# Optimization experiments

Measured on AMD Instinct MI355X. Metric: run time of the kernel, lower is better.

Reference implementation:

```python
import jax, jax.numpy as jnp
import numpy as np

B = 32
CH = 64
BAND = 16384
NOISE_SAMPLES = 64
NOISE_FRAMES = BAND // NOISE_SAMPLES          # 256
NOISE_COEFFS = NOISE_FRAMES // 2 + 1          # 129
NOISE_STEP = NOISE_FRAMES // 2                # 128


def setup_inputs() -> dict:
    key = jax.random.key(0)
    ks = jax.random.split(key, 6)
    def w(k, o, i):
        return jax.random.normal(k, (o, i), jnp.float32) / np.sqrt(i).astype(np.float32)
    x = jax.random.normal(ks[0], (B, CH, BAND), jnp.float32)
    # white noise uniform(-1, 1), generated in torch forward; here a fixed input for determinism
    white_noise = jax.random.uniform(ks[1], (B, BAND), jnp.float32) * 2.0 - 1.0
    return {
        "x": x,
        "amp_w": w(ks[2], CH, CH), "amp_b": jnp.zeros((CH,), jnp.float32),
        "freq_w": w(ks[3], CH, CH), "freq_b": jnp.zeros((CH,), jnp.float32),
        "noise_w": w(ks[4], NOISE_COEFFS, CH), "noise_b": jnp.zeros((NOISE_COEFFS,), jnp.float32),
        "noise_factor": jnp.array(1e-5, jnp.float32),
        "white_noise": white_noise,
    }


def _avg_pool_same(y, k=64, p=32):
    # F.avg_pool1d(y, 64, 1, 32)[..., :-1] with count_include_pad=True
    s = jax.lax.reduce_window(y, 0.0, jax.lax.add, (1, 1, k), (1, 1, 1),
                              ((0, 0), (0, 0), (p, p)))
    return (s / k)[..., : y.shape[-1]]


def _noise_bank2(spec, white):
    # spec: [B, M, S] per-frame rFFT magnitudes; filter white noise frame-wise, overlap-add
    b, m, s = spec.shape
    win = (m - 1) * 2          # 256
    hop = win // 2             # 128
    total = hop * s            # == BAND
    noise = jnp.pad(white, ((0, 0), (0, hop)))
    idx = jnp.arange(s)[:, None] * hop + jnp.arange(win)[None, :]
    frames = noise[:, idx]
    nf = jnp.fft.rfft(frames, norm="ortho")             # [B, S, M]
    filt = nf * jnp.transpose(spec, (0, 2, 1))          # apply magnitudes
    audio = jnp.fft.irfft(filt, n=win, norm="ortho")
    a = audio[:, :, :hop]
    tail = audio[:, :, hop:]
    ola = a.at[:, 1:, :].add(tail[:, :-1, :])
    return ola.reshape(b, 1, total)


def reference(x, amp_w, amp_b, freq_w, freq_b, noise_w, noise_b, noise_factor, white_noise):
    b, c, t = x.shape
    conv1x1 = lambda w_, b_: jnp.einsum("oc,bct->bot", w_, x) + b_[None, :, None]
    # noise branch
    n = jnp.clip(conv1x1(noise_w, noise_b), 0.0, 1.0)                 # [B, 129, T]
    n = n.reshape(b, NOISE_COEFFS, t // NOISE_STEP, NOISE_STEP).mean(-1)  # avg_pool k=s=128
    nb = _noise_bank2(n, white_noise) * noise_factor                  # [B, 1, T]
    # amp/freq oscillator branch (computed but DISCARDED by the original forward)
    amp = _avg_pool_same(jnp.clip(conv1x1(amp_w, amp_b), 0.0, 1.0))
    freq = _avg_pool_same(jnp.clip(conv1x1(freq_w, freq_b), 0.0, 1.0))
    osc = jnp.sin(jnp.cumsum(freq, axis=-1)) * amp                    # noqa: F841 (dead in source)
    out = jnp.mean(x, axis=1, keepdims=True) + nb
    return out
```

## Files before the change

### kernel.cpp

```cpp
#include <hip/hip_runtime.h>
#include <stdint.h>

#define B_    32
#define CH    64
#define T_    16384
#define NC    129
#define NFRM  128
#define QPAD  136
#define MROWS 144
#define FPB   8

typedef __attribute__((ext_vector_type(4))) float f32x4;
typedef __attribute__((ext_vector_type(4))) int   i32x4;
typedef __attribute__((ext_vector_type(8))) short bf16x8;

__device__ f32x4 llvm_amdgcn_raw_buffer_load_v4f32(i32x4 rsrc, int voffset, int soffset, int aux) __asm("llvm.amdgcn.raw.buffer.load.v4f32");

__device__ __forceinline__ unsigned short f2bs(float f) {
  union { float f; unsigned u; } v; v.f = f;
  unsigned r = (v.u + 0x7FFFu + ((v.u >> 16) & 1u)) >> 16;
  return (unsigned short)r;
}
__device__ __forceinline__ float b2f(unsigned short s) {
  union { float f; unsigned u; } v; v.u = ((unsigned)s) << 16; return v.f;
}
__device__ __forceinline__ unsigned pk2(float lo, float hi) {
  return __builtin_amdgcn_perm(__float_as_uint(hi), __float_as_uint(lo), 0x07060302u);
}
__device__ __forceinline__ i32x4 make_srsrc_wave(const void* p) {
  unsigned long long a = (unsigned long long)p;
  i32x4 r;
  r[0] = __builtin_amdgcn_readfirstlane((int)(unsigned)a);
  r[1] = __builtin_amdgcn_readfirstlane(((int)(unsigned)(a >> 32)) & 0xFFFF);
  r[2] = -1;
  r[3] = 0x00020000;
  return r;
}
__device__ __forceinline__ float dpp_sum16(float v) {
  float t;
  t = __int_as_float(__builtin_amdgcn_update_dpp(0, __float_as_int(v), 0x121, 0xF, 0xF, false)); v += t;
  t = __int_as_float(__builtin_amdgcn_update_dpp(0, __float_as_int(v), 0x122, 0xF, 0xF, false)); v += t;
  t = __int_as_float(__builtin_amdgcn_update_dpp(0, __float_as_int(v), 0x124, 0xF, 0xF, false)); v += t;
  t = __int_as_float(__builtin_amdgcn_update_dpp(0, __float_as_int(v), 0x128, 0xF, 0xF, false)); v += t;
  return v;
}
__device__ __forceinline__ void bar_lgkm() {
  asm volatile("s_waitcnt lgkmcnt(0)" ::: "memory");
  __builtin_amdgcn_s_barrier();
  asm volatile("" ::: "memory");
}

__global__ __launch_bounds__(256) void k0_setup(
    unsigned short* __restrict__ T1, unsigned short* __restrict__ T2,
    const float* __restrict__ nw, const float* __restrict__ nb,
    unsigned short* __restrict__ wb_ws, float* __restrict__ bias_ws) {
  int bid = blockIdx.x;
  if (bid < 64) {
    int g = bid * 256 + threadIdx.x;
    int base = g * 8;
    int tab = base >> 16;
    int off = base & 65535;
    int row = off >> 8, col0 = off & 255;
    const float w0 = 6.283185307179586f / 256.f;
    bf16x8 pk;
#pragma unroll
    for (int e = 0; e < 8; ++e) {
      int cq = col0 + e;
      float v;
      if (tab == 0) {
        int q = row, m = cq;
        int idx = (q <= 128) ? ((q * m) & 255) : (((q - 128) * m + 192) & 255);
        v = cosf((float)idx * w0);
      } else {
        int n = row, q = cq;
        float c = (q == 0 || q == 128) ? 1.f : 2.f;
        int idx = (q <= 128) ? ((q * n) & 255) : (((q - 128) * n + 192) & 255);
        v = c * cosf((float)idx * w0);
      }
      pk[e] = (short)f2bs(v);
    }
    *(bf16x8*)((tab ? T2 : T1) + off) = pk;
  } else {
    int t = (bid - 64) * 256 + threadIdx.x;
    if (t < MROWS * 8) {
      int q = t >> 3, o = t & 7;
      bf16x8 pk;
#pragma unroll
      for (int e = 0; e < 8; ++e) {
        unsigned short v = 0;
        if (q < NC)       v = f2bs(nw[q * 64 + o * 8 + e]);
        else if (q == 129) v = 0x3F80;
        pk[e] = (short)v;
      }
      *(bf16x8*)(wb_ws + q * 64 + o * 8) = pk;
    }
    if (t < MROWS) bias_ws[t] = (t < NC) ? nb[t] : 0.f;
  }
}

__global__ __launch_bounds__(512, 4) void k1_spec_mean(
    const float* __restrict__ x, const unsigned short* __restrict__ wb_ws,
    const float* __restrict__ bias_ws, float* __restrict__ out,
    unsigned short* __restrict__ spec_ws) {
  __shared__ __align__(16) unsigned short xbT[2][128 * 64];

  const int tid = threadIdx.x;
  const int w = tid >> 6, lane = tid & 63;
  const int l15 = lane & 15, l4 = lane >> 4;
  const int g = tid >> 5, c16 = tid & 31;
  const int b = blockIdx.y;
  const int j0 = blockIdx.x * FPB;

  const int ntile = (w == 0) ? 2 : 1;
  bf16x8 wf[2][2];
  f32x4  bfr[2];
#pragma unroll
  for (int ti = 0; ti < 2; ++ti) {
    if (ti < ntile) {
      int tile = (ti == 0) ? w : 8;
#pragma unroll
      for (int kt = 0; kt < 2; ++kt)
        wf[ti][kt] = *(const bf16x8*)(wb_ws + (tile * 16 + l15) * 64 + kt * 32 + l4 * 8);
      bfr[ti] = *(const f32x4*)(bias_ws + tile * 16 + l4 * 4);
    }
  }

  i32x4 rx = make_srsrc_wave(x + (size_t)b * CH * T_);
  const int vxbase = (g * 4 * T_ + c16 * 4) * 4;

  f32x4 r[4];
#pragma unroll
  for (int it = 0; it < 4; ++it)
    r[it] = llvm_amdgcn_raw_buffer_load_v4f32(rx, vxbase + j0 * 512, it * (T_ * 4), 0);

#pragma unroll 2
  for (int f = 0; f < FPB; ++f) {
    const int j = j0 + f;
    char* xb = (char*)xbT + (f & 1) * 16384;

    {
      const int o8 = g >> 1, h = g & 1;
#pragma unroll
      for (int e = 0; e < 4; ++e) {
        int t = c16 * 4 + e;
        unsigned a = (unsigned)(t * 128 + o8 * 16 + h * 8);
        a ^= (unsigned)(((t ^ (t >> 3)) & 7) << 4);
        uint2 dv = make_uint2(pk2(r[0][e], r[1][e]), pk2(r[2][e], r[3][e]));
        *(uint2*)(xb + a) = dv;
      }
    }
    if (f < FPB - 1) {
#pragma unroll
      for (int it = 0; it < 4; ++it)
        r[it] = llvm_amdgcn_raw_buffer_load_v4f32(rx, vxbase + (j + 1) * 512, it * (T_ * 4), 0);
    }
    bar_lgkm();

    f32x4 sum[2];
    sum[0] = (f32x4){0.f, 0.f, 0.f, 0.f};
    sum[1] = (f32x4){0.f, 0.f, 0.f, 0.f};
#pragma unroll
    for (int tt = 0; tt < 8; ++tt) {
      int t = tt * 16 + l15;
      unsigned a0 = (unsigned)(t * 128 + l4 * 16);
      a0 ^= (unsigned)(((t ^ (t >> 3)) & 7) << 4);
      bf16x8 xb0 = *(const bf16x8*)(xb + a0);
      bf16x8 xb1 = *(const bf16x8*)(xb + (a0 ^ 64));
#pragma unroll
      for (int ti = 0; ti < 2; ++ti) {
        if (ti < ntile) {
          f32x4 acc = bfr[ti];
          acc = __builtin_amdgcn_mfma_f32_16x16x32_bf16(wf[ti][0], xb0, acc, 0, 0, 0);
          acc = __builtin_amdgcn_mfma_f32_16x16x32_bf16(wf[ti][1], xb1, acc, 0, 0, 0);
          if (ti == 1 && l4 == 0)
            out[(size_t)b * T_ + (size_t)j * 128 + tt * 16 + l15] = acc[1] * (1.f / 64.f);
#pragma unroll
          for (int rr = 0; rr < 4; ++rr)
            sum[ti][rr] += __builtin_amdgcn_fmed3f(acc[rr], 0.f, 1.f);
        }
      }
    }
    unsigned short* sp = spec_ws + ((size_t)b * NFRM + j) * QPAD;
#pragma unroll
    for (int ti = 0; ti < 2; ++ti) {
      if (ti < ntile) {
        int tile = (ti == 0) ? w : 8;
        float s0 = dpp_sum16(sum[ti][0]) * (1.f / 128.f);
        float s1 = dpp_sum16(sum[ti][1]) * (1.f / 128.f);
        float s2 = dpp_sum16(sum[ti][2]) * (1.f / 128.f);
        float s3 = dpp_sum16(sum[ti][3]) * (1.f / 128.f);
        if (l15 == 0) {
          uint2 pv = make_uint2(pk2(s0, s1), pk2(s2, s3));
          *(uint2*)(sp + tile * 16 + l4 * 4) = pv;
        }
      }
    }
  }
}

__global__ __launch_bounds__(512) void k2_noise(
    const float* __restrict__ white, const unsigned short* __restrict__ spec_ws,
    const unsigned short* __restrict__ T1, const unsigned short* __restrict__ T2,
    const float* __restrict__ nf_p, float* __restrict__ out) {
  __shared__ __align__(16) unsigned short wn[4224];
  __shared__ __align__(16) unsigned short spec_l[32 * QPAD];
  __shared__ __align__(16) unsigned short G[32 * 256];
  __shared__ __align__(16) unsigned short audio[256 * 33];

  const int c = blockIdx.x, b = blockIdx.y;
  const int jb = c * 16 - 1;
  const int tid = threadIdx.x;
  const int lane = tid & 63, w = tid >> 6;
  const int l15 = lane & 15, l4 = lane >> 4;

  for (int rc = tid; rc < 528; rc += 512) {
    int g0 = jb * 128 + rc * 8;
    bf16x8 pk;
    if (rc < 288 && (unsigned)g0 < (unsigned)T_) {
      const float* wp = white + (size_t)b * T_ + g0;
      union { unsigned u[4]; bf16x8 h; } t;
#pragma unroll
      for (int p = 0; p < 4; ++p) t.u[p] = pk2(wp[2 * p], wp[2 * p + 1]);
      pk = t.h;
    } else {
#pragma unroll
      for (int e = 0; e < 8; ++e) pk[e] = 0;
    }
    unsigned a = rc * 16;
    a ^= ((a >> 8) & 7) << 4;
    *(bf16x8*)((char*)wn + a) = pk;
  }
  for (int ec = tid; ec < 32 * 17; ec += 512) {
    int s = ec / 17, cr = ec % 17;
    int jj = jb + s;
    uint4 vv = make_uint4(0u, 0u, 0u, 0u);
    if (s < 17 && (unsigned)jj < 128u)
      vv = *(const uint4*)(spec_ws + ((size_t)b * NFRM + jj) * QPAD + cr * 8);
    *(uint4*)(spec_l + s * QPAD + cr * 8) = vv;
  }
  __syncthreads();

  const f32x4 fz = {0.f, 0.f, 0.f, 0.f};
  f32x4 acc[2][2];
#pragma unroll
  for (int mi = 0; mi < 2; ++mi)
#pragma unroll
    for (int nt = 0; nt < 2; ++nt) acc[mi][nt] = fz;
#pragma unroll
  for (int kt = 0; kt < 8; ++kt) {
    bf16x8 bfr[2];
#pragma unroll
    for (int nt = 0; nt < 2; ++nt) {
      int s = nt * 16 + l15;
      unsigned a = s * 256 + kt * 64 + l4 * 16;
      a ^= ((a >> 8) & 7) << 4;
      bfr[nt] = *(const bf16x8*)((const char*)wn + a);
    }
#pragma unroll
    for (int mi = 0; mi < 2; ++mi) {
      int q = (2 * w + mi) * 16 + l15;
      bf16x8 afr = *(const bf16x8*)(T1 + q * 256 + kt * 32 + l4 * 8);
#pragma unroll
      for (int nt = 0; nt < 2; ++nt)
        acc[mi][nt] = __builtin_amdgcn_mfma_f32_16x16x32_bf16(afr, bfr[nt], acc[mi][nt], 0, 0, 0);
    }
  }
#pragma unroll
  for (int mi = 0; mi < 2; ++mi) {
    int qbase = (2 * w + mi) * 16 + l4 * 4;
#pragma unroll
    for (int nt = 0; nt < 2; ++nt) {
      int s = nt * 16 + l15;
#pragma unroll
      for (int rp = 0; rp < 2; ++rp) {
        int q0 = qbase + rp * 2;
        int kk0 = (q0 <= 128) ? q0 : q0 - 128;
        int kk1 = (q0 + 1 <= 128) ? q0 + 1 : q0 - 127;
        float s0 = b2f(spec_l[s * QPAD + kk0]);
        float s1 = b2f(spec_l[s * QPAD + kk1]);
        unsigned pw = pk2(acc[mi][nt][rp * 2] * s0, acc[mi][nt][rp * 2 + 1] * s1);
        unsigned a = s * 512 + q0 * 2;
        a ^= ((a >> 9) & 7) << 4;
        *(unsigned*)((char*)G + a) = pw;
      }
    }
  }
  __syncthreads();

  f32x4 acc2[2][2];
#pragma unroll
  for (int mi = 0; mi < 2; ++mi)
#pragma unroll
    for (int nt = 0; nt < 2; ++nt) acc2[mi][nt] = fz;
#pragma unroll
  for (int kt = 0; kt < 8; ++kt) {
    bf16x8 bfr[2];
#pragma unroll
    for (int nt = 0; nt < 2; ++nt) {
      int s = nt * 16 + l15;
      unsigned a = s * 512 + kt * 64 + l4 * 16;
      a ^= ((a >> 9) & 7) << 4;
      bfr[nt] = *(const bf16x8*)((const char*)G + a);
    }
#pragma unroll
    for (int mi = 0; mi < 2; ++mi) {
      int n = (2 * w + mi) * 16 + l15;
      bf16x8 afr = *(const bf16x8*)(T2 + n * 256 + kt * 32 + l4 * 8);
#pragma unroll
      for (int nt = 0; nt < 2; ++nt)
        acc2[mi][nt] = __builtin_amdgcn_mfma_f32_16x16x32_bf16(afr, bfr[nt], acc2[mi][nt], 0, 0, 0);
    }
  }
#pragma unroll
  for (int mi = 0; mi < 2; ++mi)
#pragma unroll
    for (int nt = 0; nt < 2; ++nt)
#pragma unroll
      for (int r = 0; r < 4; ++r) {
        int n = (2 * w + mi) * 16 + l4 * 4 + r;
        int s = nt * 16 + l15;
        audio[n * 33 + s] = f2bs(acc2[mi][nt][r]);
      }
  __syncthreads();

  const float cf = nf_p[0] * (1.f / 256.f);
  {
    int t0 = tid * 4;
    int n = t0 & 127, jl = t0 >> 7;
    int s1 = jl + 1;
    size_t o = (size_t)b * T_ + (size_t)c * 2048 + t0;
    f32x4 ov = *(f32x4*)(out + o);
#pragma unroll
    for (int e = 0; e < 4; ++e) {
      float a1 = b2f(audio[(n + e) * 33 + s1]);
      float a2 = b2f(audio[(n + e + 128) * 33 + jl]);
      ov[e] += cf * (a1 + a2);
    }
    *(f32x4*)(out + o) = ov;
  }
}

extern "C" void kernel_launch(void* const* d_in, const int* in_sizes, int n_in,
                              void* d_out, int out_size, void* d_ws, size_t ws_size,
                              hipStream_t stream) {
  (void)in_sizes; (void)n_in; (void)out_size; (void)ws_size;
  const float* x            = (const float*)d_in[0];
  const float* noise_w      = (const float*)d_in[5];
  const float* noise_b      = (const float*)d_in[6];
  const float* noise_factor = (const float*)d_in[7];
  const float* white        = (const float*)d_in[8];
  float* out = (float*)d_out;

  unsigned short* T1    = (unsigned short*)d_ws;
  unsigned short* T2    = T1 + 65536;
  unsigned short* spec  = T2 + 65536;
  unsigned short* wb_ws = spec + (size_t)B_ * NFRM * QPAD;
  float*          bias_ws = (float*)(wb_ws + MROWS * 64);

  k0_setup<<<69, 256, 0, stream>>>(T1, T2, noise_w, noise_b, wb_ws, bias_ws);
  k1_spec_mean<<<dim3(NFRM / FPB, B_), 512, 0, stream>>>(x, wb_ws, bias_ws, out, spec);
  k2_noise<<<dim3(8, B_), 512, 0, stream>>>(white, spec, T1, T2, noise_factor, out);
}
```

Measured before the change: 44.82 us.

## Halve k2 chunk size for more blocks and deepen k1 prefetch to two frames

The noise kernel now processes 8 frames per block instead of 16, which doubles the grid to 512 blocks and shrinks shared memory and per-wave accumulators to one N tile. The aim is better occupancy and spreading across CUs, at the cost of reloading more T1/T2 table fragments and the one-frame halo per block. The spec/mean kernel is fully unrolled with two register buffers so global loads for x are issued two frames ahead, hiding more load latency at the cost of higher register pressure.

```diff
diff --git a/kernel.cpp b/kernel.cpp
--- a/kernel.cpp
+++ b/kernel.cpp
@@ -9,6 +9,7 @@
 #define QPAD  136
 #define MROWS 144
 #define FPB   8
+#define CHK   8
 
 typedef __attribute__((ext_vector_type(4))) float f32x4;
 typedef __attribute__((ext_vector_type(4))) int   i32x4;
@@ -88,7 +89,7 @@
 #pragma unroll
       for (int e = 0; e < 8; ++e) {
         unsigned short v = 0;
-        if (q < NC)       v = f2bs(nw[q * 64 + o * 8 + e]);
+        if (q < NC)        v = f2bs(nw[q * 64 + o * 8 + e]);
         else if (q == 129) v = 0x3F80;
         pk[e] = (short)v;
       }
@@ -127,96 +128,110 @@
 
   i32x4 rx = make_srsrc_wave(x + (size_t)b * CH * T_);
   const int vxbase = (g * 4 * T_ + c16 * 4) * 4;
-
-  f32x4 r[4];
+  const int o8 = g >> 1, hh = g & 1;
+
+  f32x4 rA[4], rB[4];
 #pragma unroll
   for (int it = 0; it < 4; ++it)
-    r[it] = llvm_amdgcn_raw_buffer_load_v4f32(rx, vxbase + j0 * 512, it * (T_ * 4), 0);
-
-#pragma unroll 2
-  for (int f = 0; f < FPB; ++f) {
-    const int j = j0 + f;
-    char* xb = (char*)xbT + (f & 1) * 16384;
-
-    {
-      const int o8 = g >> 1, h = g & 1;
-#pragma unroll
-      for (int e = 0; e < 4; ++e) {
-        int t = c16 * 4 + e;
-        unsigned a = (unsigned)(t * 128 + o8 * 16 + h * 8);
-        a ^= (unsigned)(((t ^ (t >> 3)) & 7) << 4);
-        uint2 dv = make_uint2(pk2(r[0][e], r[1][e]), pk2(r[2][e], r[3][e]));
-        *(uint2*)(xb + a) = dv;
-      }
-    }
-    if (f < FPB - 1) {
-#pragma unroll
-      for (int it = 0; it < 4; ++it)
-        r[it] = llvm_amdgcn_raw_buffer_load_v4f32(rx, vxbase + (j + 1) * 512, it * (T_ * 4), 0);
-    }
-    bar_lgkm();
-
-    f32x4 sum[2];
-    sum[0] = (f32x4){0.f, 0.f, 0.f, 0.f};
-    sum[1] = (f32x4){0.f, 0.f, 0.f, 0.f};
-#pragma unroll
-    for (int tt = 0; tt < 8; ++tt) {
-      int t = tt * 16 + l15;
-      unsigned a0 = (unsigned)(t * 128 + l4 * 16);
-      a0 ^= (unsigned)(((t ^ (t >> 3)) & 7) << 4);
-      bf16x8 xb0 = *(const bf16x8*)(xb + a0);
-      bf16x8 xb1 = *(const bf16x8*)(xb + (a0 ^ 64));
-#pragma unroll
-      for (int ti = 0; ti < 2; ++ti) {
-        if (ti < ntile) {
-          f32x4 acc = bfr[ti];
-          acc = __builtin_amdgcn_mfma_f32_16x16x32_bf16(wf[ti][0], xb0, acc, 0, 0, 0);
-          acc = __builtin_amdgcn_mfma_f32_16x16x32_bf16(wf[ti][1], xb1, acc, 0, 0, 0);
-          if (ti == 1 && l4 == 0)
-            out[(size_t)b * T_ + (size_t)j * 128 + tt * 16 + l15] = acc[1] * (1.f / 64.f);
-#pragma unroll
-          for (int rr = 0; rr < 4; ++rr)
-            sum[ti][rr] += __builtin_amdgcn_fmed3f(acc[rr], 0.f, 1.f);
-        }
-      }
-    }
-    unsigned short* sp = spec_ws + ((size_t)b * NFRM + j) * QPAD;
-#pragma unroll
-    for (int ti = 0; ti < 2; ++ti) {
-      if (ti < ntile) {
-        int tile = (ti == 0) ? w : 8;
-        float s0 = dpp_sum16(sum[ti][0]) * (1.f / 128.f);
-        float s1 = dpp_sum16(sum[ti][1]) * (1.f / 128.f);
-        float s2 = dpp_sum16(sum[ti][2]) * (1.f / 128.f);
-        float s3 = dpp_sum16(sum[ti][3]) * (1.f / 128.f);
-        if (l15 == 0) {
-          uint2 pv = make_uint2(pk2(s0, s1), pk2(s2, s3));
-          *(uint2*)(sp + tile * 16 + l4 * 4) = pv;
-        }
-      }
-    }
-  }
+    rA[it] = llvm_amdgcn_raw_buffer_load_v4f32(rx, vxbase + j0 * 512, it * (T_ * 4), 0);
+#pragma unroll
+  for (int it = 0; it < 4; ++it)
+    rB[it] = llvm_amdgcn_raw_buffer_load_v4f32(rx, vxbase + (j0 + 1) * 512, it * (T_ * 4), 0);
+
+#define K1_FRAME(F, R)                                                        \
+  {                                                                           \
+    const int j = j0 + (F);                                                   \
+    char* xb = (char*)xbT + ((F) & 1) * 16384;                                \
+    _Pragma("unroll")                                                         \
+    for (int e = 0; e < 4; ++e) {                                             \
+      int t = c16 * 4 + e;                                                    \
+      unsigned a = (unsigned)(t * 128 + o8 * 16 + hh * 8);                    \
+      a ^= (unsigned)(((t ^ (t >> 3)) & 7) << 4);                             \
+      uint2 dv = make_uint2(pk2(R[0][e], R[1][e]), pk2(R[2][e], R[3][e]));    \
+      *(uint2*)(xb + a) = dv;                                                 \
+    }                                                                         \
+    if ((F) + 2 < FPB) {                                                      \
+      _Pragma("unroll")                                                       \
+      for (int it = 0; it < 4; ++it)                                          \
+        R[it] = llvm_amdgcn_raw_buffer_load_v4f32(rx, vxbase + (j + 2) * 512, \
+                                                  it * (T_ * 4), 0);          \
+    }                                                                         \
+    bar_lgkm();                                                               \
+    f32x4 sum0 = {0.f, 0.f, 0.f, 0.f};                                        \
+    f32x4 sum1 = {0.f, 0.f, 0.f, 0.f};                                        \
+    _Pragma("unroll")                                                         \
+    for (int tt = 0; tt < 8; ++tt) {                                          \
+      int t = tt * 16 + l15;                                                  \
+      unsigned a0 = (unsigned)(t * 128 + l4 * 16);                            \
+      a0 ^= (unsigned)(((t ^ (t >> 3)) & 7) << 4);                            \
+      bf16x8 xb0 = *(const bf16x8*)(xb + a0);                                 \
+      bf16x8 xb1 = *(const bf16x8*)(xb + (a0 ^ 64));                          \
+      {                                                                       \
+        f32x4 acc = bfr[0];                                                   \
+        acc = __builtin_amdgcn_mfma_f32_16x16x32_bf16(wf[0][0], xb0, acc, 0, 0, 0); \
+        acc = __builtin_amdgcn_mfma_f32_16x16x32_bf16(wf[0][1], xb1, acc, 0, 0, 0); \
+        _Pragma("unroll")                                                     \
+        for (int rr = 0; rr < 4; ++rr)                                        \
+          sum0[rr] += __builtin_amdgcn_fmed3f(acc[rr], 0.f, 1.f);             \
+      }                                                                       \
+      if (ntile == 2) {                                                       \
+        f32x4 acc = bfr[1];                                                   \
+        acc = __builtin_amdgcn_mfma_f32_16x16x32_bf16(wf[1][0], xb0, acc, 0, 0, 0); \
+        acc = __builtin_amdgcn_mfma_f32_16x16x32_bf16(wf[1][1], xb1, acc, 0, 0, 0); \
+        if (l4 == 0)                                                          \
+          out[(size_t)b * T_ + (size_t)j * 128 + tt * 16 + l15] = acc[1] * (1.f / 64.f); \
+        _Pragma("unroll")                                                     \
+        for (int rr = 0; rr < 4; ++rr)                                        \
+          sum1[rr] += __builtin_amdgcn_fmed3f(acc[rr], 0.f, 1.f);             \
+      }                                                                       \
+    }                                                                         \
+    unsigned short* sp = spec_ws + ((size_t)b * NFRM + j) * QPAD;             \
+    {                                                                         \
+      float s0 = dpp_sum16(sum0[0]) * (1.f / 128.f);                          \
+      float s1 = dpp_sum16(sum0[1]) * (1.f / 128.f);                          \
+      float s2 = dpp_sum16(sum0[2]) * (1.f / 128.f);                          \
+      float s3 = dpp_sum16(sum0[3]) * (1.f / 128.f);                          \
+      if (l15 == 0) {                                                         \
+        uint2 pv = make_uint2(pk2(s0, s1), pk2(s2, s3));                      \
+        *(uint2*)(sp + w * 16 + l4 * 4) = pv;                                 \
+      }                                                                       \
+    }                                                                         \
+    if (ntile == 2) {                                                         \
+      float s0 = dpp_sum16(sum1[0]) * (1.f / 128.f);                          \
+      float s1 = dpp_sum16(sum1[1]) * (1.f / 128.f);                          \
+      float s2 = dpp_sum16(sum1[2]) * (1.f / 128.f);                          \
+      float s3 = dpp_sum16(sum1[3]) * (1.f / 128.f);                          \
+      if (l15 == 0) {                                                         \
+        uint2 pv = make_uint2(pk2(s0, s1), pk2(s2, s3));                      \
+        *(uint2*)(sp + 8 * 16 + l4 * 4) = pv;                                 \
+      }                                                                       \
+    }                                                                         \
+  }
+
+  K1_FRAME(0, rA) K1_FRAME(1, rB) K1_FRAME(2, rA) K1_FRAME(3, rB)
+  K1_FRAME(4, rA) K1_FRAME(5, rB) K1_FRAME(6, rA) K1_FRAME(7, rB)
+#undef K1_FRAME
 }
 
 __global__ __launch_bounds__(512) void k2_noise(
     const float* __restrict__ white, const unsigned short* __restrict__ spec_ws,
     const unsigned short* __restrict__ T1, const unsigned short* __restrict__ T2,
     const float* __restrict__ nf_p, float* __restrict__ out) {
-  __shared__ __align__(16) unsigned short wn[4224];
-  __shared__ __align__(16) unsigned short spec_l[32 * QPAD];
-  __shared__ __align__(16) unsigned short G[32 * 256];
-  __shared__ __align__(16) unsigned short audio[256 * 33];
+  __shared__ __align__(16) unsigned short wn[2304];
+  __shared__ __align__(16) unsigned short spec_l[16 * QPAD];
+  __shared__ __align__(16) unsigned short G[16 * 256];
+  __shared__ __align__(16) unsigned short audio[256 * 17];
 
   const int c = blockIdx.x, b = blockIdx.y;
-  const int jb = c * 16 - 1;
+  const int jb = c * CHK - 1;
   const int tid = threadIdx.x;
   const int lane = tid & 63, w = tid >> 6;
   const int l15 = lane & 15, l4 = lane >> 4;
 
-  for (int rc = tid; rc < 528; rc += 512) {
+  for (int rc = tid; rc < 288; rc += 512) {
     int g0 = jb * 128 + rc * 8;
     bf16x8 pk;
-    if (rc < 288 && (unsigned)g0 < (unsigned)T_) {
+    if (rc < 160 && (unsigned)g0 < (unsigned)T_) {
       const float* wp = white + (size_t)b * T_ + g0;
       union { unsigned u[4]; bf16x8 h; } t;
 #pragma unroll
@@ -230,113 +245,81 @@
     a ^= ((a >> 8) & 7) << 4;
     *(bf16x8*)((char*)wn + a) = pk;
   }
-  for (int ec = tid; ec < 32 * 17; ec += 512) {
+  for (int ec = tid; ec < 16 * 17; ec += 512) {
     int s = ec / 17, cr = ec % 17;
     int jj = jb + s;
     uint4 vv = make_uint4(0u, 0u, 0u, 0u);
-    if (s < 17 && (unsigned)jj < 128u)
+    if (s < CHK + 1 && (unsigned)jj < 128u)
       vv = *(const uint4*)(spec_ws + ((size_t)b * NFRM + jj) * QPAD + cr * 8);
     *(uint4*)(spec_l + s * QPAD + cr * 8) = vv;
   }
   __syncthreads();
 
   const f32x4 fz = {0.f, 0.f, 0.f, 0.f};
-  f32x4 acc[2][2];
-#pragma unroll
-  for (int mi = 0; mi < 2; ++mi)
-#pragma unroll
-    for (int nt = 0; nt < 2; ++nt) acc[mi][nt] = fz;
+  f32x4 acc[2] = {fz, fz};
 #pragma unroll
   for (int kt = 0; kt < 8; ++kt) {
-    bf16x8 bfr[2];
-#pragma unroll
-    for (int nt = 0; nt < 2; ++nt) {
-      int s = nt * 16 + l15;
-      unsigned a = s * 256 + kt * 64 + l4 * 16;
-      a ^= ((a >> 8) & 7) << 4;
-      bfr[nt] = *(const bf16x8*)((const char*)wn + a);
-    }
+    unsigned a = l15 * 256 + kt * 64 + l4 * 16;
+    a ^= ((a >> 8) & 7) << 4;
+    bf16x8 bfr = *(const bf16x8*)((const char*)wn + a);
 #pragma unroll
     for (int mi = 0; mi < 2; ++mi) {
       int q = (2 * w + mi) * 16 + l15;
       bf16x8 afr = *(const bf16x8*)(T1 + q * 256 + kt * 32 + l4 * 8);
-#pragma unroll
-      for (int nt = 0; nt < 2; ++nt)
-        acc[mi][nt] = __builtin_amdgcn_mfma_f32_16x16x32_bf16(afr, bfr[nt], acc[mi][nt], 0, 0, 0);
+      acc[mi] = __builtin_amdgcn_mfma_f32_16x16x32_bf16(afr, bfr, acc[mi], 0, 0, 0);
     }
   }
 #pragma unroll
   for (int mi = 0; mi < 2; ++mi) {
     int qbase = (2 * w + mi) * 16 + l4 * 4;
-#pragma unroll
-    for (int nt = 0; nt < 2; ++nt) {
-      int s = nt * 16 + l15;
-#pragma unroll
-      for (int rp = 0; rp < 2; ++rp) {
-        int q0 = qbase + rp * 2;
-        int kk0 = (q0 <= 128) ? q0 : q0 - 128;
-        int kk1 = (q0 + 1 <= 128) ? q0 + 1 : q0 - 127;
-        float s0 = b2f(spec_l[s * QPAD + kk0]);
-        float s1 = b2f(spec_l[s * QPAD + kk1]);
-        unsigned pw = pk2(acc[mi][nt][rp * 2] * s0, acc[mi][nt][rp * 2 + 1] * s1);
-        unsigned a = s * 512 + q0 * 2;
-        a ^= ((a >> 9) & 7) << 4;
-        *(unsigned*)((char*)G + a) = pw;
-      }
+    int s = l15;
+#pragma unroll
+    for (int rp = 0; rp < 2; ++rp) {
+      int q0 = qbase + rp * 2;
+      int kk0 = (q0 <= 128) ? q0 : q0 - 128;
+      int kk1 = (q0 + 1 <= 128) ? q0 + 1 : q0 - 127;
+      float s0 = b2f(spec_l[s * QPAD + kk0]);
+      float s1 = b2f(spec_l[s * QPAD + kk1]);
+      unsigned pw = pk2(acc[mi][rp * 2] * s0, acc[mi][rp * 2 + 1] * s1);
+      unsigned a = s * 512 + q0 * 2;
+      a ^= ((a >> 9) & 7) << 4;
+      *(unsigned*)((char*)G + a) = pw;
     }
   }
   __syncthreads();
 
-  f32x4 acc2[2][2];
-#pragma unroll
-  for (int mi = 0; mi < 2; ++mi)
-#pragma unroll
-    for (int nt = 0; nt < 2; ++nt) acc2[mi][nt] = fz;
+  f32x4 acc2[2] = {fz, fz};
 #pragma unroll
   for (int kt = 0; kt < 8; ++kt) {
-    bf16x8 bfr[2];
-#pragma unroll
-    for (int nt = 0; nt < 2; ++nt) {
-      int s = nt * 16 + l15;
-      unsigned a = s * 512 + kt * 64 + l4 * 16;
-      a ^= ((a >> 9) & 7) << 4;
-      bfr[nt] = *(const bf16x8*)((const char*)G + a);
-    }
+    unsigned a = l15 * 512 + kt * 64 + l4 * 16;
+    a ^= ((a >> 9) & 7) << 4;
+    bf16x8 bfr = *(const bf16x8*)((const char*)G + a);
 #pragma unroll
     for (int mi = 0; mi < 2; ++mi) {
       int n = (2 * w + mi) * 16 + l15;
       bf16x8 afr = *(const bf16x8*)(T2 + n * 256 + kt * 32 + l4 * 8);
-#pragma unroll
-      for (int nt = 0; nt < 2; ++nt)
-        acc2[mi][nt] = __builtin_amdgcn_mfma_f32_16x16x32_bf16(afr, bfr[nt], acc2[mi][nt], 0, 0, 0);
+      acc2[mi] = __builtin_amdgcn_mfma_f32_16x16x32_bf16(afr, bfr, acc2[mi], 0, 0, 0);
     }
   }
 #pragma unroll
   for (int mi = 0; mi < 2; ++mi)
 #pragma unroll
-    for (int nt = 0; nt < 2; ++nt)
-#pragma unroll
-      for (int r = 0; r < 4; ++r) {
-        int n = (2 * w + mi) * 16 + l4 * 4 + r;
-        int s = nt * 16 + l15;
-        audio[n * 33 + s] = f2bs(acc2[mi][nt][r]);
-      }
+    for (int r = 0; r < 4; ++r) {
+      int n = (2 * w + mi) * 16 + l4 * 4 + r;
+      audio[n * 17 + l15] = f2bs(acc2[mi][r]);
+    }
   __syncthreads();
 
   const float cf = nf_p[0] * (1.f / 256.f);
   {
-    int t0 = tid * 4;
-    int n = t0 & 127, jl = t0 >> 7;
+    int i = tid * 2;
+    int n = i & 127, jl = i >> 7;
     int s1 = jl + 1;
-    size_t o = (size_t)b * T_ + (size_t)c * 2048 + t0;
-    f32x4 ov = *(f32x4*)(out + o);
-#pragma unroll
-    for (int e = 0; e < 4; ++e) {
-      float a1 = b2f(audio[(n + e) * 33 + s1]);
-      float a2 = b2f(audio[(n + e + 128) * 33 + jl]);
-      ov[e] += cf * (a1 + a2);
-    }
-    *(f32x4*)(out + o) = ov;
+    size_t o = (size_t)b * T_ + (size_t)c * (CHK * 128) + i;
+    float2 ov = *(float2*)(out + o);
+    ov.x += cf * (b2f(audio[n * 17 + s1]) + b2f(audio[(n + 128) * 17 + jl]));
+    ov.y += cf * (b2f(audio[(n + 1) * 17 + s1]) + b2f(audio[(n + 129) * 17 + jl]));
+    *(float2*)(out + o) = ov;
   }
 }
 
@@ -359,5 +342,5 @@
 
   k0_setup<<<69, 256, 0, stream>>>(T1, T2, noise_w, noise_b, wb_ws, bias_ws);
   k1_spec_mean<<<dim3(NFRM / FPB, B_), 512, 0, stream>>>(x, wb_ws, bias_ws, out, spec);
-  k2_noise<<<dim3(8, B_), 512, 0, stream>>>(white, spec, T1, T2, noise_factor, out);
-}
+  k2_noise<<<dim3(T_ / (CHK * 128), B_), 512, 0, stream>>>(white, spec, T1, T2, noise_factor, out);
+}
```

Result: slower. 54.82 us (+22.3%).
